# Performance work log

Measured on AMD Instinct MI355X. Metric: run time of the kernel, lower is better.

The kernel has to match this reference:

```python
import jax, jax.numpy as jnp
import numpy as np

B, L, D, H = 2, 256, 512, 8
DV = D // H
INF = 1e12

def _xavier(key, shape, fan_in, fan_out):
    a = float(np.sqrt(6.0 / (fan_in + fan_out)))
    return jax.random.uniform(key, shape, minval=-a, maxval=a, dtype=jnp.float32)

def setup_inputs() -> dict:
    key = jax.random.key(0)
    ks = jax.random.split(key, 9)
    inp = jax.random.normal(ks[0], (B, L, D), dtype=jnp.float32)
    relation_inp = jax.random.normal(ks[1], (B, L, L, D), dtype=jnp.float32)
    mask = jax.random.randint(ks[2], (B, L, L), 0, 2).astype(bool)
    adj_mask = jax.random.randint(ks[3], (B, H, L, L), 0, 2).astype(jnp.float32)
    W_value = _xavier(ks[4], (D, H * DV), D, H * DV)
    W_relation = _xavier(ks[5], (D, H * DV), D, H * DV)
    # weight vectors have torch shape (1,1,1,H,DV); xavier fans over last two dims
    w_src = _xavier(ks[6], (H, DV), H, DV)
    w_tgt = _xavier(ks[7], (H, DV), H, DV)
    w_rel = _xavier(ks[8], (H, DV), H, DV)
    return {"inp": inp, "relation_inp": relation_inp, "mask": mask,
            "adj_mask": adj_mask, "W_value": W_value, "W_relation": W_relation,
            "w_src": w_src, "w_tgt": w_tgt, "w_rel": w_rel}

def reference(inp, relation_inp, mask, adj_mask, W_value, W_relation, w_src, w_tgt, w_rel):
    b, l, d = inp.shape
    h, dv = w_src.shape
    # value: (B,H,L,DV)
    value = (inp @ W_value).reshape(b, l, h, dv).transpose(0, 2, 1, 3)
    # relation: (B,L,L,H,DV)
    relation = (relation_inp @ W_relation).reshape(b, l, l, h, dv)
    # scores[b,h,i,j] = w_src.v_j + w_tgt.v_i + w_rel.rel[b,i,j,h]
    s_src = jnp.einsum('bhjd,hd->bhj', value, w_src)[:, :, None, :]
    s_tgt = jnp.einsum('bhid,hd->bhi', value, w_tgt)[:, :, :, None]
    s_rel = jnp.einsum('bijhd,hd->bhij', relation, w_rel)
    scores = s_src + s_tgt + s_rel
    scores = jnp.where(scores >= 0, scores, 0.2 * scores)  # LeakyReLU(0.2)
    m = mask[:, None]  # (B,1,L,L)
    adj_zero = adj_mask == 0
    scores = jnp.where(m, -INF, scores)
    scores = jnp.where(adj_zero, -INF, scores)
    attn = jax.nn.softmax(scores, axis=-1)
    # normalized: divide by edge weight (zeros -> weight INF -> 1/INF)
    inv = jnp.where(adj_zero, 1.0 / INF, 1.0 / jnp.where(adj_zero, 1.0, adj_mask))
    attn = attn * inv
    attn = attn / jnp.maximum(jnp.sum(jnp.abs(attn), axis=-1, keepdims=True), 1e-12)
    attn = jnp.where(m, 0.0, attn)
    attn = jnp.where(adj_zero, 0.0, attn)
    out = jnp.einsum('bhij,bhjd->bhid', attn, value)
    out = out.transpose(0, 2, 1, 3).reshape(b, l, d)  # concat heads
    return out + inp
```

## Files before the change

### kernel.cpp

```cpp
#include <hip/hip_runtime.h>

#define B_ 2
#define L_ 256
#define D_ 512
#define H_ 8
#define DV_ 64
#define NEGINF 1e12f

#define WS_VALUE 0
#define WS_WR    262144
#define WS_SSRC  266240
#define WS_STGT  270336

__global__ __launch_bounds__(256) void k_wr(const float* __restrict__ Wrel,
                                            const float* __restrict__ wrel,
                                            float* __restrict__ WR) {
    int flat = blockIdx.x * 256 + threadIdx.x;
    int k = flat >> 3, h = flat & 7;
    const float* a = Wrel + k * 512 + h * 64;
    const float* b = wrel + h * 64;
    float s = 0.f;
#pragma unroll
    for (int d = 0; d < 64; d += 4) {
        float4 x = *(const float4*)(a + d);
        float4 y = *(const float4*)(b + d);
        s += x.x * y.x + x.y * y.y + x.z * y.z + x.w * y.w;
    }
    WR[k * 8 + h] = s;
}

__global__ __launch_bounds__(256) void k_value(const float* __restrict__ inp,
                                               const float* __restrict__ Wv,
                                               float* __restrict__ value) {
    int blk = blockIdx.x;
    int ct  = blk & 1;
    int rt  = blk >> 1;
    int n   = ct * 256 + threadIdx.x;
    int r0  = rt * 4;
    const float* i0 = inp + (size_t)(r0 + 0) * 512;
    const float* i1 = inp + (size_t)(r0 + 1) * 512;
    const float* i2 = inp + (size_t)(r0 + 2) * 512;
    const float* i3 = inp + (size_t)(r0 + 3) * 512;
    float a0 = 0.f, a1 = 0.f, a2 = 0.f, a3 = 0.f;
#pragma unroll 8
    for (int k = 0; k < 512; ++k) {
        float w = Wv[(size_t)k * 512 + n];
        a0 = fmaf(i0[k], w, a0);
        a1 = fmaf(i1[k], w, a1);
        a2 = fmaf(i2[k], w, a2);
        a3 = fmaf(i3[k], w, a3);
    }
    int h = n >> 6, dv = n & 63;
    float acc[4] = {a0, a1, a2, a3};
#pragma unroll
    for (int r = 0; r < 4; ++r) {
        int row = r0 + r;
        int b = row >> 8, l = row & 255;
        value[(((size_t)(b * 8 + h)) * 256 + l) * 64 + dv] = acc[r];
    }
}

__global__ __launch_bounds__(256) void k_src_tgt(const float* __restrict__ value,
                                                 const float* __restrict__ wsrc,
                                                 const float* __restrict__ wtgt,
                                                 float* __restrict__ s_src,
                                                 float* __restrict__ s_tgt) {
    int flat = blockIdx.x * 256 + threadIdx.x;
    int h = (flat >> 8) & 7;
    const float* v  = value + (size_t)flat * 64;
    const float* ws = wsrc + h * 64;
    const float* wt = wtgt + h * 64;
    float ss = 0.f, st = 0.f;
#pragma unroll
    for (int d = 0; d < 64; d += 4) {
        float4 x = *(const float4*)(v + d);
        float4 s4 = *(const float4*)(ws + d);
        float4 t4 = *(const float4*)(wt + d);
        ss += x.x * s4.x + x.y * s4.y + x.z * s4.z + x.w * s4.w;
        st += x.x * t4.x + x.y * t4.y + x.z * t4.z + x.w * t4.w;
    }
    s_src[flat] = ss;
    s_tgt[flat] = st;
}

__global__ __launch_bounds__(256) void k_main(const float* __restrict__ rel,
                                              const int*   __restrict__ mask,
                                              const float* __restrict__ adj,
                                              const float* __restrict__ inp,
                                              const float* __restrict__ value,
                                              const float* __restrict__ WR,
                                              const float* __restrict__ s_src,
                                              const float* __restrict__ s_tgt,
                                              float* __restrict__ out) {
    __shared__ float tile[256 * 64];
    int bi  = blockIdx.x;
    int b   = bi >> 8;
    int i   = bi & 255;
    int tid = threadIdx.x;

    float acc[8];
#pragma unroll
    for (int h = 0; h < 8; ++h) acc[h] = 0.f;

    const float* relbase = rel + (size_t)bi * 256 * 512;

    for (int kt = 0; kt < 8; ++kt) {
        int k0 = kt * 64;
#pragma unroll
        for (int ii = 0; ii < 16; ++ii) {
            int f = ii * 256 + tid;
            int r = f >> 4;
            int c = f & 15;
            float4 v = *(const float4*)(relbase + (size_t)r * 512 + k0 + c * 4);
            int w = r * 64 + ((c ^ (r & 15)) << 2);
            *(float4*)&tile[w] = v;
        }
        __syncthreads();

        const float* wrt = WR + k0 * 8;
#pragma unroll
        for (int c = 0; c < 16; ++c) {
            float4 x = *(const float4*)&tile[tid * 64 + ((c ^ (tid & 15)) << 2)];
#pragma unroll
            for (int h = 0; h < 8; ++h) {
                acc[h] = fmaf(x.x, wrt[(c * 4 + 0) * 8 + h],
                         fmaf(x.y, wrt[(c * 4 + 1) * 8 + h],
                         fmaf(x.z, wrt[(c * 4 + 2) * 8 + h],
                         fmaf(x.w, wrt[(c * 4 + 3) * 8 + h], acc[h]))));
            }
        }
        __syncthreads();
    }

    float* srel_s = tile;
    float* attn_s = tile + 2048;
#pragma unroll
    for (int h = 0; h < 8; ++h) srel_s[h * 256 + tid] = acc[h];
    __syncthreads();

    {
        int h  = tid >> 5;
        int ln = tid & 31;
        float stgt = s_tgt[(size_t)(b * 8 + h) * 256 + i];
        const float* ssrc   = s_src + (size_t)(b * 8 + h) * 256;
        const float* adjrow = adj + ((size_t)(b * 8 + h) * 256 + i) * 256;
        const int*   mrow   = mask + (size_t)bi * 256;

        float sc[8], av[8];
        int mb = 0;
        float rowmax = -3.0e38f;
#pragma unroll
        for (int t = 0; t < 8; ++t) {
            int j = ln + 32 * t;
            float a = adjrow[j];
            av[t] = a;
            int m = mrow[j];
            float s = ssrc[j] + stgt + srel_s[h * 256 + j];
            s = (s >= 0.f) ? s : 0.2f * s;
            if (m != 0) { s = -NEGINF; mb |= (1 << t); }
            if (a == 0.f) s = -NEGINF;
            sc[t] = s;
            rowmax = fmaxf(rowmax, s);
        }
#pragma unroll
        for (int off = 16; off >= 1; off >>= 1)
            rowmax = fmaxf(rowmax, __shfl_xor(rowmax, off));

        float rowsum = 0.f;
#pragma unroll
        for (int t = 0; t < 8; ++t) {
            sc[t] = expf(sc[t] - rowmax);
            rowsum += sc[t];
        }
#pragma unroll
        for (int off = 16; off >= 1; off >>= 1)
            rowsum += __shfl_xor(rowsum, off);

        float sumabs = 0.f;
#pragma unroll
        for (int t = 0; t < 8; ++t) {
            float p = sc[t] / rowsum;
            float invv = (av[t] == 0.f) ? 1e-12f : (1.0f / av[t]);
            p *= invv;
            sc[t] = p;
            sumabs += fabsf(p);
        }
#pragma unroll
        for (int off = 16; off >= 1; off >>= 1)
            sumabs += __shfl_xor(sumabs, off);

        float rdn = 1.0f / fmaxf(sumabs, 1e-12f);
#pragma unroll
        for (int t = 0; t < 8; ++t) {
            float p = sc[t] * rdn;
            if (mb & (1 << t)) p = 0.f;
            if (av[t] == 0.f) p = 0.f;
            attn_s[h * 256 + ln + 32 * t] = p;
        }
    }
    __syncthreads();

    {
        int h  = tid >> 5;
        int d0 = (tid & 31) * 2;
        const float* vbase = value + ((size_t)(b * 8 + h) * 256) * 64 + d0;
        const float* arow  = attn_s + h * 256;
        float ax = 0.f, ay = 0.f;
#pragma unroll 4
        for (int j = 0; j < 256; ++j) {
            float a = arow[j];
            float2 v2 = *(const float2*)(vbase + (size_t)j * 64);
            ax = fmaf(a, v2.x, ax);
            ay = fmaf(a, v2.y, ay);
        }
        size_t o = (size_t)bi * 512 + h * 64 + d0;
        out[o]     = inp[o] + ax;
        out[o + 1] = inp[o + 1] + ay;
    }
}

extern "C" void kernel_launch(void* const* d_in, const int* in_sizes, int n_in,
                              void* d_out, int out_size, void* d_ws, size_t ws_size,
                              hipStream_t stream) {
    const float* inp      = (const float*)d_in[0];
    const float* rel      = (const float*)d_in[1];
    const int*   mask     = (const int*)  d_in[2];
    const float* adj      = (const float*)d_in[3];
    const float* W_value  = (const float*)d_in[4];
    const float* W_rel    = (const float*)d_in[5];
    const float* w_src    = (const float*)d_in[6];
    const float* w_tgt    = (const float*)d_in[7];
    const float* w_rel    = (const float*)d_in[8];
    float* out = (float*)d_out;

    float* ws    = (float*)d_ws;
    float* value = ws + WS_VALUE;
    float* WR    = ws + WS_WR;
    float* s_src = ws + WS_SSRC;
    float* s_tgt = ws + WS_STGT;

    k_wr<<<16, 256, 0, stream>>>(W_rel, w_rel, WR);
    k_value<<<256, 256, 0, stream>>>(inp, W_value, value);
    k_src_tgt<<<16, 256, 0, stream>>>(value, w_src, w_tgt, s_src, s_tgt);
    k_main<<<B_ * L_, 256, 0, stream>>>(rel, mask, adj, inp, value, WR,
                                        s_src, s_tgt, out);
}
```

Baseline: 114.8 us.

## Double-buffer relation tiles via direct global-to-LDS loads in main kernel

The relation-score loop in the main kernel now fetches 32-column tiles straight into LDS with global_load_lds and double buffers them. The next tile is prefetched while the current one is consumed, using vmcnt waits in place of block-wide barriers. Each wave loads only the rows it later reads, so the per-tile __syncthreads are dropped. This targets the exposed latency of streaming the large relation tensor, at the cost of relying on hand-written waitcnt ordering. The value projection loop's unroll factor is also raised from 8 to 16.

```diff
diff --git a/kernel.cpp b/kernel.cpp
--- a/kernel.cpp
+++ b/kernel.cpp
@@ -11,6 +11,11 @@
 #define WS_WR    262144
 #define WS_SSRC  266240
 #define WS_STGT  270336
+
+#define GLOAD_LDS16(g, l)                                                     \
+    __builtin_amdgcn_global_load_lds(                                         \
+        (const __attribute__((address_space(1))) void*)(g),                   \
+        (__attribute__((address_space(3))) void*)(l), 16, 0, 0)
 
 __global__ __launch_bounds__(256) void k_wr(const float* __restrict__ Wrel,
                                             const float* __restrict__ wrel,
@@ -42,7 +47,7 @@
     const float* i2 = inp + (size_t)(r0 + 2) * 512;
     const float* i3 = inp + (size_t)(r0 + 3) * 512;
     float a0 = 0.f, a1 = 0.f, a2 = 0.f, a3 = 0.f;
-#pragma unroll 8
+#pragma unroll 16
     for (int k = 0; k < 512; ++k) {
         float w = Wv[(size_t)k * 512 + n];
         a0 = fmaf(i0[k], w, a0);
@@ -92,48 +97,68 @@
                                               const float* __restrict__ s_src,
                                               const float* __restrict__ s_tgt,
                                               float* __restrict__ out) {
-    __shared__ float tile[256 * 64];
-    int bi  = blockIdx.x;
-    int b   = bi >> 8;
-    int i   = bi & 255;
-    int tid = threadIdx.x;
+    __shared__ float lds[16384];
+    int bi   = blockIdx.x;
+    int b    = bi >> 8;
+    int i    = bi & 255;
+    int tid  = threadIdx.x;
+    int w    = tid >> 6;
+    int lane = tid & 63;
+
+    const float* relbase = rel + (size_t)bi * 256 * 512;
+
+    const float* gsrc[8];
+    {
+#pragma unroll
+        for (int s = 0; s < 8; ++s) {
+            int f = w * 512 + s * 64 + lane;
+            int r = f >> 3, c = f & 7;
+            int cp = c ^ (r & 7);
+            gsrc[s] = relbase + (size_t)r * 512 + cp * 4;
+        }
+    }
+
+#define STAGE(bufofs, k0)                                                      \
+    {                                                                          \
+        _Pragma("unroll")                                                      \
+        for (int s = 0; s < 8; ++s)                                            \
+            GLOAD_LDS16(gsrc[s] + (k0), &lds[(bufofs) + w * 2048 + s * 256]);  \
+    }
 
     float acc[8];
 #pragma unroll
     for (int h = 0; h < 8; ++h) acc[h] = 0.f;
 
-    const float* relbase = rel + (size_t)bi * 256 * 512;
-
-    for (int kt = 0; kt < 8; ++kt) {
-        int k0 = kt * 64;
-#pragma unroll
-        for (int ii = 0; ii < 16; ++ii) {
-            int f = ii * 256 + tid;
-            int r = f >> 4;
-            int c = f & 15;
-            float4 v = *(const float4*)(relbase + (size_t)r * 512 + k0 + c * 4);
-            int w = r * 64 + ((c ^ (r & 15)) << 2);
-            *(float4*)&tile[w] = v;
-        }
-        __syncthreads();
-
-        const float* wrt = WR + k0 * 8;
-#pragma unroll
-        for (int c = 0; c < 16; ++c) {
-            float4 x = *(const float4*)&tile[tid * 64 + ((c ^ (tid & 15)) << 2)];
+    int tswz = tid & 7;
+
+    STAGE(0, 0);
+    for (int kt = 0; kt < 16; ++kt) {
+        int cur = (kt & 1) * 8192;
+        if (kt < 15) {
+            int nxt = ((kt + 1) & 1) * 8192;
+            STAGE(nxt, (kt + 1) * 32);
+            asm volatile("s_waitcnt vmcnt(8)" ::: "memory");
+        } else {
+            asm volatile("s_waitcnt vmcnt(0)" ::: "memory");
+        }
+        const float* myrow = &lds[cur + tid * 32];
+        const float* wrt   = WR + kt * 32 * 8;
+#pragma unroll
+        for (int q = 0; q < 8; ++q) {
+            float4 x = *(const float4*)&myrow[(q ^ tswz) << 2];
 #pragma unroll
             for (int h = 0; h < 8; ++h) {
-                acc[h] = fmaf(x.x, wrt[(c * 4 + 0) * 8 + h],
-                         fmaf(x.y, wrt[(c * 4 + 1) * 8 + h],
-                         fmaf(x.z, wrt[(c * 4 + 2) * 8 + h],
-                         fmaf(x.w, wrt[(c * 4 + 3) * 8 + h], acc[h]))));
+                acc[h] = fmaf(x.x, wrt[(q * 4 + 0) * 8 + h],
+                         fmaf(x.y, wrt[(q * 4 + 1) * 8 + h],
+                         fmaf(x.z, wrt[(q * 4 + 2) * 8 + h],
+                         fmaf(x.w, wrt[(q * 4 + 3) * 8 + h], acc[h]))));
             }
         }
-        __syncthreads();
-    }
-
-    float* srel_s = tile;
-    float* attn_s = tile + 2048;
+    }
+
+    __syncthreads();
+    float* srel_s = lds;
+    float* attn_s = lds + 2048;
 #pragma unroll
     for (int h = 0; h < 8; ++h) srel_s[h * 256 + tid] = acc[h];
     __syncthreads();
```

Measured after the change: 123.6 us. 1.08x slower.

## Skip loading masked relation rows and fuse src/tgt scores into value GEMM

Applied to the files above, without the earlier changes.

The main kernel builds a compacted list of unmasked columns with a ballot/prefix scan and only streams those relation rows from memory, since masked scores are overwritten with -INF anyway. This cuts the dominant relation-tensor traffic roughly in proportion to the mask density. The s_src/s_tgt dot products are fused into the value projection kernel using wave shuffle reductions, removing one launch. Minor unroll changes and a reciprocal-multiply replace a division; the gather adds an indirection and a pre-pass sync.

```diff
diff --git a/kernel.cpp b/kernel.cpp
--- a/kernel.cpp
+++ b/kernel.cpp
@@ -31,7 +31,11 @@
 
 __global__ __launch_bounds__(256) void k_value(const float* __restrict__ inp,
                                                const float* __restrict__ Wv,
-                                               float* __restrict__ value) {
+                                               const float* __restrict__ wsrc,
+                                               const float* __restrict__ wtgt,
+                                               float* __restrict__ value,
+                                               float* __restrict__ s_src,
+                                               float* __restrict__ s_tgt) {
     int blk = blockIdx.x;
     int ct  = blk & 1;
     int rt  = blk >> 1;
@@ -42,7 +46,7 @@
     const float* i2 = inp + (size_t)(r0 + 2) * 512;
     const float* i3 = inp + (size_t)(r0 + 3) * 512;
     float a0 = 0.f, a1 = 0.f, a2 = 0.f, a3 = 0.f;
-#pragma unroll 8
+#pragma unroll 16
     for (int k = 0; k < 512; ++k) {
         float w = Wv[(size_t)k * 512 + n];
         a0 = fmaf(i0[k], w, a0);
@@ -52,35 +56,25 @@
     }
     int h = n >> 6, dv = n & 63;
     float acc[4] = {a0, a1, a2, a3};
+    float wsv = wsrc[h * 64 + dv];
+    float wtv = wtgt[h * 64 + dv];
 #pragma unroll
     for (int r = 0; r < 4; ++r) {
         int row = r0 + r;
         int b = row >> 8, l = row & 255;
         value[(((size_t)(b * 8 + h)) * 256 + l) * 64 + dv] = acc[r];
-    }
-}
-
-__global__ __launch_bounds__(256) void k_src_tgt(const float* __restrict__ value,
-                                                 const float* __restrict__ wsrc,
-                                                 const float* __restrict__ wtgt,
-                                                 float* __restrict__ s_src,
-                                                 float* __restrict__ s_tgt) {
-    int flat = blockIdx.x * 256 + threadIdx.x;
-    int h = (flat >> 8) & 7;
-    const float* v  = value + (size_t)flat * 64;
-    const float* ws = wsrc + h * 64;
-    const float* wt = wtgt + h * 64;
-    float ss = 0.f, st = 0.f;
-#pragma unroll
-    for (int d = 0; d < 64; d += 4) {
-        float4 x = *(const float4*)(v + d);
-        float4 s4 = *(const float4*)(ws + d);
-        float4 t4 = *(const float4*)(wt + d);
-        ss += x.x * s4.x + x.y * s4.y + x.z * s4.z + x.w * s4.w;
-        st += x.x * t4.x + x.y * t4.y + x.z * t4.z + x.w * t4.w;
-    }
-    s_src[flat] = ss;
-    s_tgt[flat] = st;
+        float ss = acc[r] * wsv;
+        float st = acc[r] * wtv;
+#pragma unroll
+        for (int off = 32; off >= 1; off >>= 1) {
+            ss += __shfl_xor(ss, off);
+            st += __shfl_xor(st, off);
+        }
+        if (dv == 0) {
+            s_src[(size_t)(b * 8 + h) * 256 + l] = ss;
+            s_tgt[(size_t)(b * 8 + h) * 256 + l] = st;
+        }
+    }
 }
 
 __global__ __launch_bounds__(256) void k_main(const float* __restrict__ rel,
@@ -93,40 +87,64 @@
                                               const float* __restrict__ s_tgt,
                                               float* __restrict__ out) {
     __shared__ float tile[256 * 64];
-    int bi  = blockIdx.x;
-    int b   = bi >> 8;
-    int i   = bi & 255;
-    int tid = threadIdx.x;
+    __shared__ int   list_s[256];
+    __shared__ int   wavecnt[4];
+    __shared__ int   count_s;
+    int bi   = blockIdx.x;
+    int b    = bi >> 8;
+    int i    = bi & 255;
+    int tid  = threadIdx.x;
+    int lane = tid & 63;
+    int wv   = tid >> 6;
+
+    const int* mrow = mask + (size_t)bi * 256;
+    int mymask = mrow[tid];
+    unsigned long long vote = __ballot(mymask == 0);
+    int prefix = __popcll(vote & ((1ull << lane) - 1ull));
+    if (lane == 0) wavecnt[wv] = __popcll(vote);
+    __syncthreads();
+    int base = 0;
+    for (int wq = 0; wq < wv; ++wq) base += wavecnt[wq];
+    if (mymask == 0) list_s[base + prefix] = tid;
+    if (tid == 0) count_s = wavecnt[0] + wavecnt[1] + wavecnt[2] + wavecnt[3];
+    __syncthreads();
+    int count = count_s;
 
     float acc[8];
 #pragma unroll
     for (int h = 0; h < 8; ++h) acc[h] = 0.f;
 
     const float* relbase = rel + (size_t)bi * 256 * 512;
+    int nf    = count * 16;
+    int niter = (nf + 255) >> 8;
 
     for (int kt = 0; kt < 8; ++kt) {
         int k0 = kt * 64;
-#pragma unroll
-        for (int ii = 0; ii < 16; ++ii) {
+        for (int ii = 0; ii < niter; ++ii) {
             int f = ii * 256 + tid;
-            int r = f >> 4;
-            int c = f & 15;
-            float4 v = *(const float4*)(relbase + (size_t)r * 512 + k0 + c * 4);
-            int w = r * 64 + ((c ^ (r & 15)) << 2);
-            *(float4*)&tile[w] = v;
+            if (f < nf) {
+                int r = f >> 4;
+                int c = f & 15;
+                int row = list_s[r];
+                float4 v = *(const float4*)(relbase + (size_t)row * 512 + k0 + c * 4);
+                int wd = r * 64 + ((c ^ (r & 15)) << 2);
+                *(float4*)&tile[wd] = v;
+            }
         }
         __syncthreads();
 
-        const float* wrt = WR + k0 * 8;
-#pragma unroll
-        for (int c = 0; c < 16; ++c) {
-            float4 x = *(const float4*)&tile[tid * 64 + ((c ^ (tid & 15)) << 2)];
-#pragma unroll
-            for (int h = 0; h < 8; ++h) {
-                acc[h] = fmaf(x.x, wrt[(c * 4 + 0) * 8 + h],
-                         fmaf(x.y, wrt[(c * 4 + 1) * 8 + h],
-                         fmaf(x.z, wrt[(c * 4 + 2) * 8 + h],
-                         fmaf(x.w, wrt[(c * 4 + 3) * 8 + h], acc[h]))));
+        if (tid < count) {
+            const float* wrt = WR + k0 * 8;
+#pragma unroll
+            for (int c = 0; c < 16; ++c) {
+                float4 x = *(const float4*)&tile[tid * 64 + ((c ^ (tid & 15)) << 2)];
+#pragma unroll
+                for (int h = 0; h < 8; ++h) {
+                    acc[h] = fmaf(x.x, wrt[(c * 4 + 0) * 8 + h],
+                             fmaf(x.y, wrt[(c * 4 + 1) * 8 + h],
+                             fmaf(x.z, wrt[(c * 4 + 2) * 8 + h],
+                             fmaf(x.w, wrt[(c * 4 + 3) * 8 + h], acc[h]))));
+                }
             }
         }
         __syncthreads();
@@ -134,8 +152,11 @@
 
     float* srel_s = tile;
     float* attn_s = tile + 2048;
-#pragma unroll
-    for (int h = 0; h < 8; ++h) srel_s[h * 256 + tid] = acc[h];
+    if (tid < count) {
+        int row = list_s[tid];
+#pragma unroll
+        for (int h = 0; h < 8; ++h) srel_s[h * 256 + row] = acc[h];
+    }
     __syncthreads();
 
     {
@@ -144,7 +165,6 @@
         float stgt = s_tgt[(size_t)(b * 8 + h) * 256 + i];
         const float* ssrc   = s_src + (size_t)(b * 8 + h) * 256;
         const float* adjrow = adj + ((size_t)(b * 8 + h) * 256 + i) * 256;
-        const int*   mrow   = mask + (size_t)bi * 256;
 
         float sc[8], av[8];
         int mb = 0;
@@ -175,11 +195,12 @@
 #pragma unroll
         for (int off = 16; off >= 1; off >>= 1)
             rowsum += __shfl_xor(rowsum, off);
+        float rinv = 1.0f / rowsum;
 
         float sumabs = 0.f;
 #pragma unroll
         for (int t = 0; t < 8; ++t) {
-            float p = sc[t] / rowsum;
+            float p = sc[t] * rinv;
             float invv = (av[t] == 0.f) ? 1e-12f : (1.0f / av[t]);
             p *= invv;
             sc[t] = p;
@@ -206,7 +227,7 @@
         const float* vbase = value + ((size_t)(b * 8 + h) * 256) * 64 + d0;
         const float* arow  = attn_s + h * 256;
         float ax = 0.f, ay = 0.f;
-#pragma unroll 4
+#pragma unroll 8
         for (int j = 0; j < 256; ++j) {
             float a = arow[j];
             float2 v2 = *(const float2*)(vbase + (size_t)j * 64);
@@ -240,8 +261,8 @@
     float* s_tgt = ws + WS_STGT;
 
     k_wr<<<16, 256, 0, stream>>>(W_rel, w_rel, WR);
-    k_value<<<256, 256, 0, stream>>>(inp, W_value, value);
-    k_src_tgt<<<16, 256, 0, stream>>>(value, w_src, w_tgt, s_src, s_tgt);
+    k_value<<<256, 256, 0, stream>>>(inp, W_value, w_src, w_tgt,
+                                     value, s_src, s_tgt);
     k_main<<<B_ * L_, 256, 0, stream>>>(rel, mask, adj, inp, value, WR,
                                         s_src, s_tgt, out);
 }
```

Result: no change. 115.3 us (+0.5%).
